# Kernel optimization log

Measured on AMD Instinct MI355X. Metric: run time of the kernel, lower is better.

Reference implementation:

```python
import jax, jax.numpy as jnp
import numpy as np

B, K, L, D, H, DFF, E = 4, 1024, 32, 128, 8, 512, 16384


def setup_inputs() -> dict:
    key = jax.random.key(0)
    ks = jax.random.split(key, 16)
    p = lambda k, sh: (jax.random.normal(k, sh, jnp.float32) * 0.02)
    return {
        "x": jax.random.normal(ks[0], (B, K, L, D), jnp.float32),
        "edge_index": jax.random.randint(ks[1], (B, 2, E), 0, K, jnp.int32),
        "edge_weight": jax.random.uniform(ks[2], (B, E), jnp.float32),
        "w_qkv": p(ks[3], (3 * D, D)), "b_qkv": p(ks[4], (3 * D,)),
        "w_out": p(ks[5], (D, D)), "b_out": p(ks[6], (D,)),
        "w1": p(ks[7], (DFF, D)), "b1": p(ks[8], (DFF,)),
        "w2": p(ks[9], (D, DFF)), "b2": p(ks[10], (D,)),
        "ln1_g": jnp.ones((D,), jnp.float32), "ln1_b": jnp.zeros((D,), jnp.float32),
        "ln2_g": jnp.ones((D,), jnp.float32), "ln2_b": jnp.zeros((D,), jnp.float32),
        "gcn_w": p(ks[11], (D, D)), "gcn_b": p(ks[12], (D,)),
    }


def _ln(x, g, b, eps=1e-5):
    m = x.mean(-1, keepdims=True)
    v = ((x - m) ** 2).mean(-1, keepdims=True)
    return (x - m) * jax.lax.rsqrt(v + eps) * g + b


def reference(x, edge_index, edge_weight, w_qkv, b_qkv, w_out, b_out,
              w1, b1, w2, b2, ln1_g, ln1_b, ln2_g, ln2_b, gcn_w, gcn_b):
    Bx, Kx, Lx, Dx = x.shape
    dh = Dx // H
    h = x.reshape(Bx * Kx, Lx, Dx)                       # [N, L, D], N = B*K
    # --- post-norm TransformerEncoderLayer (self-attn + FFN, relu, dropout=0) ---
    qkv = h @ w_qkv.T + b_qkv
    q, k_, v = jnp.split(qkv, 3, axis=-1)
    q = q.reshape(-1, Lx, H, dh)
    k_ = k_.reshape(-1, Lx, H, dh)
    v = v.reshape(-1, Lx, H, dh)
    scores = jnp.einsum('nlhd,nmhd->nhlm', q, k_) / np.float32(np.sqrt(dh))
    attn = jax.nn.softmax(scores, axis=-1)
    o = jnp.einsum('nhlm,nmhd->nlhd', attn, v).reshape(-1, Lx, Dx)
    o = o @ w_out.T + b_out
    h = _ln(h + o, ln1_g, ln1_b)
    ff = jax.nn.relu(h @ w1.T + b1) @ w2.T + b2
    h = _ln(h + ff, ln2_g, ln2_b)
    xt = h.reshape(Bx, Kx, Lx, Dx)
    # --- GCNConv (sym-normalized, self-loops) applied per (b, l) slice; batched over L ---
    self_idx = jnp.arange(Kx, dtype=edge_index.dtype)

    def gcn_one(xb, ei, ew):                              # xb [K, L, D]
        hh = xb @ gcn_w.T                                 # X W
        row = jnp.concatenate([ei[0], self_idx])          # sources (+ self loops)
        col = jnp.concatenate([ei[1], self_idx])          # targets
        w = jnp.concatenate([ew, jnp.ones((Kx,), ew.dtype)])
        deg = jax.ops.segment_sum(w, col, num_segments=Kx)
        deg_safe = jnp.where(deg > 0, deg, 1.0)
        dinv = jnp.where(deg > 0, jax.lax.rsqrt(deg_safe), 0.0)
        norm = dinv[row] * w * dinv[col]                  # [E+K]
        msg = hh[row] * norm[:, None, None]               # gather + scale
        return jax.ops.segment_sum(msg, col, num_segments=Kx) + gcn_b

    g = jax.vmap(gcn_one)(xt, edge_index, edge_weight)
    return xt + g
```

## Files before the change

kernel.cpp:

```cpp
#include <hip/hip_runtime.h>
#include <hip/hip_bf16.h>

#define BDIM 4
#define KDIM 1024
#define EDIM 16384
#define NSEQ (BDIM * KDIM)
#define REG  25856
#define MOFF 9216

typedef unsigned short ushort_t;
typedef unsigned int   uint32;

typedef __bf16 bf16x8 __attribute__((ext_vector_type(8)));
typedef float  f32x4  __attribute__((ext_vector_type(4)));

#define MFMA(A, B, C) __builtin_amdgcn_mfma_f32_16x16x32_bf16((A), (B), (C), 0, 0, 0)
#define PRIO_HI() __builtin_amdgcn_s_setprio(1)
#define PRIO_LO() __builtin_amdgcn_s_setprio(0)

__device__ __forceinline__ float bf2f(uint32 u) {
    union { uint32 i; float f; } v; v.i = u << 16; return v.f;
}
__device__ __forceinline__ ushort_t f2bf(float f) {
    union { float f; uint32 i; } v; v.f = f;
    uint32 r = (v.i + 0x7fffu + ((v.i >> 16) & 1u)) >> 16;
    return (ushort_t)r;
}
__device__ __forceinline__ uint32 cvtpk(float a, float b) {
    uint32 r;
    asm("v_cvt_pk_bf16_f32 %0, %1, %2" : "=v"(r) : "v"(a), "v"(b));
    return r;
}
__device__ __forceinline__ ushort_t f2bf_hw(float f) { return (ushort_t)cvtpk(f, f); }

__device__ __forceinline__ void unpack8(uint4 v, float* dst) {
    const uint32* pv = (const uint32*)&v;
#pragma unroll
    for (int q = 0; q < 4; q++) {
        uint32 w = pv[q];
        dst[2 * q]     = bf2f(w & 0xffffu);
        dst[2 * q + 1] = bf2f(w >> 16);
    }
}
__device__ __forceinline__ void store16bf(ushort_t* p, const float* v) {
    uint32 w[8];
#pragma unroll
    for (int q = 0; q < 8; q++) w[q] = cvtpk(v[2 * q], v[2 * q + 1]);
    ((uint4*)p)[0] = make_uint4(w[0], w[1], w[2], w[3]);
    ((uint4*)p)[1] = make_uint4(w[4], w[5], w[6], w[7]);
}

#define NWCVT 212992
__global__ void k_prep(const float* __restrict__ wq, const float* __restrict__ wo,
                       const float* __restrict__ w1, const float* __restrict__ w2,
                       const float* __restrict__ wg, ushort_t* __restrict__ dst,
                       float* __restrict__ deg, int* __restrict__ count) {
    int i = blockIdx.x * 256 + threadIdx.x;
    if (i >= NWCVT) return;
    if (i < BDIM * KDIM) { deg[i] = 1.0f; count[i] = 0; }
    float v;
    if      (i <  49152) v = wq[i];
    else if (i <  65536) v = wo[i - 49152];
    else if (i < 131072) v = w1[i - 65536];
    else if (i < 196608) v = w2[i - 131072];
    else                 v = wg[i - 196608];
    dst[i] = f2bf(v);
}

__global__ __launch_bounds__(256)
void k_transformer(const float* __restrict__ x,
                   const ushort_t* __restrict__ wq_bf, const float* __restrict__ b_qkv,
                   const ushort_t* __restrict__ wo_bf, const float* __restrict__ b_out,
                   const ushort_t* __restrict__ w1_bf, const float* __restrict__ b1,
                   const ushort_t* __restrict__ w2_bf, const float* __restrict__ b2,
                   const ushort_t* __restrict__ wg_bf,
                   const float* __restrict__ ln1g, const float* __restrict__ ln1b,
                   const float* __restrict__ ln2g, const float* __restrict__ ln2b,
                   float* __restrict__ out_xt, ushort_t* __restrict__ hh)
{
    const int n0   = blockIdx.x * 2;
    const int tid  = threadIdx.x;
    const int wave = tid >> 6;
    const int lane = tid & 63;
    const int lh   = lane & 15;
    const int lg   = lane >> 4;
    const int l    = tid >> 3;
    const int ds   = (tid & 7) * 16;

    __shared__ __align__(16) char smem[2 * REG];
#define SH(s)  ((ushort_t*)(smem + (s) * REG))
#define SVT(s) ((ushort_t*)(smem + (s) * REG))
#define SM(s)  ((ushort_t*)(smem + (s) * REG + MOFF))
#define SMF(s) ((float*)(smem + (s) * REG + MOFF))

#pragma unroll
    for (int s = 0; s < 2; s++) {
        const float4* px = (const float4*)(x + (size_t)(n0 + s) * 4096 + tid * 16);
        float h0[16];
#pragma unroll
        for (int q = 0; q < 4; q++) {
            float4 v = px[q];
            h0[4 * q] = v.x; h0[4 * q + 1] = v.y; h0[4 * q + 2] = v.z; h0[4 * q + 3] = v.w;
        }
        store16bf(SH(s) + l * 136 + ds, h0);
    }
    __syncthreads();

    {
        bf16x8 af[2][2][4];
#pragma unroll
        for (int s = 0; s < 2; s++)
#pragma unroll
            for (int mt = 0; mt < 2; mt++)
#pragma unroll
                for (int kk = 0; kk < 4; kk++)
                    af[s][mt][kk] = *(const bf16x8*)(SH(s) + (mt * 16 + lh) * 136 + kk * 32 + lg * 8);
        __syncthreads();

        const int ntb = wave * 6;
        float biasv[6];
#pragma unroll
        for (int j = 0; j < 6; j++) biasv[j] = b_qkv[(ntb + j) * 16 + lh];
#pragma unroll
        for (int j = 0; j < 6; j++) {
            bf16x8 bw[4];
#pragma unroll
            for (int kk = 0; kk < 4; kk++)
                bw[kk] = *(const bf16x8*)(wq_bf + (size_t)((ntb + j) * 16 + lh) * 128 + kk * 32 + lg * 8);
            f32x4 A[2][2];
#pragma unroll
            for (int s = 0; s < 2; s++) { A[s][0] = f32x4{0.f,0.f,0.f,0.f}; A[s][1] = f32x4{0.f,0.f,0.f,0.f}; }
            PRIO_HI();
#pragma unroll
            for (int kk = 0; kk < 4; kk++) {
#pragma unroll
                for (int s = 0; s < 2; s++) {
                    A[s][0] = MFMA(af[s][0][kk], bw[kk], A[s][0]);
                    A[s][1] = MFMA(af[s][1][kk], bw[kk], A[s][1]);
                }
            }
            PRIO_LO();
            const int nt  = ntb + j;
            const int col = nt * 16 + lh;
            const float bias = biasv[j];
#pragma unroll
            for (int s = 0; s < 2; s++) {
                if (nt < 16) {
                    const int r0 = lg * 4;
#pragma unroll
                    for (int i = 0; i < 4; i++) {
                        SM(s)[(r0 + i) * 260 + col]      = f2bf_hw(A[s][0][i] + bias);
                        SM(s)[(16 + r0 + i) * 260 + col] = f2bf_hw(A[s][1][i] + bias);
                    }
                } else {
                    const int vc = col - 256;
                    uint32 p01 = cvtpk(A[s][0][0] + bias, A[s][0][1] + bias);
                    uint32 p23 = cvtpk(A[s][0][2] + bias, A[s][0][3] + bias);
                    uint32 q01 = cvtpk(A[s][1][0] + bias, A[s][1][1] + bias);
                    uint32 q23 = cvtpk(A[s][1][2] + bias, A[s][1][3] + bias);
                    *(uint32*)&SVT(s)[vc * 36 + lg * 4]          = p01;
                    *(uint32*)&SVT(s)[vc * 36 + lg * 4 + 2]      = p23;
                    *(uint32*)&SVT(s)[vc * 36 + 16 + lg * 4]     = q01;
                    *(uint32*)&SVT(s)[vc * 36 + 16 + lg * 4 + 2] = q23;
                }
            }
        }
    }
    __syncthreads();

    {
        bf16x8 wbo[2][4];
#pragma unroll
        for (int j = 0; j < 2; j++)
#pragma unroll
            for (int kk = 0; kk < 4; kk++)
                wbo[j][kk] = *(const bf16x8*)(wo_bf + (size_t)((wave * 2 + j) * 16 + lh) * 128 + kk * 32 + lg * 8);
        float bo0 = b_out[(wave * 2 + 0) * 16 + lh];
        float bo1 = b_out[(wave * 2 + 1) * 16 + lh];

#pragma unroll
        for (int s = 0; s < 2; s++) {
            f32x4 sA[2][2][2];
            bf16x8 bz = {};
            PRIO_HI();
#pragma unroll
            for (int hd = 0; hd < 2; hd++) {
                const int h8 = wave * 2 + hd;
#pragma unroll
                for (int mt = 0; mt < 2; mt++) {
                    bf16x8 aq = *(const bf16x8*)(SM(s) + (mt * 16 + lh) * 260 + h8 * 16 + (lg & 1) * 8);
#pragma unroll
                    for (int nt = 0; nt < 2; nt++) {
                        bf16x8 bk = bz;
                        if (lg < 2)
                            bk = *(const bf16x8*)(SM(s) + (nt * 16 + lh) * 260 + 128 + h8 * 16 + lg * 8);
                        f32x4 z = {0.f,0.f,0.f,0.f};
                        sA[hd][mt][nt] = MFMA(aq, bk, z);
                    }
                }
            }
            PRIO_LO();
#pragma unroll
            for (int hd = 0; hd < 2; hd++) {
                const int cb = hd ? (128 + wave * 32) : (wave * 32);
#pragma unroll
                for (int mt = 0; mt < 2; mt++) {
#pragma unroll
                    for (int i = 0; i < 4; i++) {
                        float e0 = __expf(sA[hd][mt][0][i] * 0.25f);
                        float e1 = __expf(sA[hd][mt][1][i] * 0.25f);
                        float sm = e0 + e1;
                        sm += __shfl_xor(sm, 1); sm += __shfl_xor(sm, 2);
                        sm += __shfl_xor(sm, 4); sm += __shfl_xor(sm, 8);
                        float inv = 1.0f / sm;
                        const int row = mt * 16 + lg * 4 + i;
                        SM(s)[row * 260 + cb + lh]      = f2bf_hw(e0 * inv);
                        SM(s)[row * 260 + cb + 16 + lh] = f2bf_hw(e1 * inv);
                    }
                }
            }
            PRIO_HI();
#pragma unroll
            for (int hd = 0; hd < 2; hd++) {
                const int h8 = wave * 2 + hd;
                const int cb = hd ? (128 + wave * 32) : (wave * 32);
                bf16x8 bv = *(const bf16x8*)(SVT(s) + (h8 * 16 + lh) * 36 + lg * 8);
#pragma unroll
                for (int mt = 0; mt < 2; mt++) {
                    bf16x8 ap = *(const bf16x8*)(SM(s) + (mt * 16 + lh) * 260 + cb + lg * 8);
                    f32x4 z = {0.f,0.f,0.f,0.f};
                    f32x4 o = MFMA(ap, bv, z);
                    const int r0 = mt * 16 + lg * 4, c = h8 * 16 + lh;
#pragma unroll
                    for (int i = 0; i < 4; i++)
                        SM(s)[(r0 + i) * 260 + c] = f2bf_hw(o[i]);
                }
            }
            PRIO_LO();
        }
        __syncthreads();
#pragma unroll
        for (int s = 0; s < 2; s++) {
            bf16x8 af2[2][4];
#pragma unroll
            for (int mt = 0; mt < 2; mt++)
#pragma unroll
                for (int kk = 0; kk < 4; kk++)
                    af2[mt][kk] = *(const bf16x8*)(SM(s) + (mt * 16 + lh) * 260 + kk * 32 + lg * 8);
#pragma unroll
            for (int j = 0; j < 2; j++) {
                f32x4 a0 = {0.f,0.f,0.f,0.f}, a1 = {0.f,0.f,0.f,0.f};
                PRIO_HI();
#pragma unroll
                for (int kk = 0; kk < 4; kk++) {
                    a0 = MFMA(af2[0][kk], wbo[j][kk], a0);
                    a1 = MFMA(af2[1][kk], wbo[j][kk], a1);
                }
                PRIO_LO();
                const int col = (wave * 2 + j) * 16 + lh;
                const float bias = j ? bo1 : bo0;
#pragma unroll
                for (int i = 0; i < 4; i++) {
                    SH(s)[(lg * 4 + i) * 136 + col]      = f2bf_hw(a0[i] + bias);
                    SH(s)[(16 + lg * 4 + i) * 136 + col] = f2bf_hw(a1[i] + bias);
                }
            }
        }
        __syncthreads();
        {
            float g[16], be[16];
            {
                const float4* pg = (const float4*)(ln1g + ds);
                const float4* pb = (const float4*)(ln1b + ds);
#pragma unroll
                for (int q = 0; q < 4; q++) {
                    float4 vg = pg[q], vb = pb[q];
                    g[4*q]=vg.x; g[4*q+1]=vg.y; g[4*q+2]=vg.z; g[4*q+3]=vg.w;
                    be[4*q]=vb.x; be[4*q+1]=vb.y; be[4*q+2]=vb.z; be[4*q+3]=vb.w;
                }
            }
#pragma unroll
            for (int s = 0; s < 2; s++) {
                const float4* px = (const float4*)(x + (size_t)(n0 + s) * 4096 + tid * 16);
                float4 hx0 = px[0], hx1 = px[1], hx2 = px[2], hx3 = px[3];
                float h0v[16];
                { float4 v = hx0; h0v[0]=v.x; h0v[1]=v.y; h0v[2]=v.z; h0v[3]=v.w; }
                { float4 v = hx1; h0v[4]=v.x; h0v[5]=v.y; h0v[6]=v.z; h0v[7]=v.w; }
                { float4 v = hx2; h0v[8]=v.x; h0v[9]=v.y; h0v[10]=v.z; h0v[11]=v.w; }
                { float4 v = hx3; h0v[12]=v.x; h0v[13]=v.y; h0v[14]=v.z; h0v[15]=v.w; }
                float t[16]; float sum = 0.f;
#pragma unroll
                for (int i = 0; i < 16; i++) {
                    t[i] = h0v[i] + bf2f((uint32)SH(s)[l * 136 + ds + i]);
                    sum += t[i];
                }
                sum += __shfl_xor(sum, 1); sum += __shfl_xor(sum, 2); sum += __shfl_xor(sum, 4);
                float mean = sum * (1.f / 128.f);
                float vs = 0.f;
#pragma unroll
                for (int i = 0; i < 16; i++) { float d = t[i] - mean; vs += d * d; }
                vs += __shfl_xor(vs, 1); vs += __shfl_xor(vs, 2); vs += __shfl_xor(vs, 4);
                float rs = rsqrtf(vs * (1.f / 128.f) + 1e-5f);
                float h1v[16];
#pragma unroll
                for (int i = 0; i < 16; i++)
                    h1v[i] = (t[i] - mean) * rs * g[i] + be[i];
                store16bf(SH(s) + l * 136 + ds, h1v);
            }
        }
    }
    __syncthreads();

    f32x4 fa[2][4];
#pragma unroll
    for (int s = 0; s < 2; s++)
#pragma unroll
        for (int q = 0; q < 4; q++) fa[s][q] = f32x4{0.f,0.f,0.f,0.f};
    const int col0 = wave * 32 + lh, col1 = col0 + 16;
#pragma unroll
    for (int r = 0; r < 2; r++) {
#pragma unroll
        for (int s = 0; s < 2; s++) {
            bf16x8 ah[2][4];
#pragma unroll
            for (int mt = 0; mt < 2; mt++)
#pragma unroll
                for (int kk = 0; kk < 4; kk++)
                    ah[mt][kk] = *(const bf16x8*)(SH(s) + (mt * 16 + lh) * 136 + kk * 32 + lg * 8);
            float b1v[4];
#pragma unroll
            for (int j = 0; j < 4; j++) b1v[j] = b1[(r * 16 + wave * 4 + j) * 16 + lh];
#pragma unroll
            for (int j = 0; j < 4; j++) {
                bf16x8 bw[4];
                {
                    const int nt = (r * 16 + wave * 4 + j) * 16 + lh;
#pragma unroll
                    for (int kk = 0; kk < 4; kk++)
                        bw[kk] = *(const bf16x8*)(w1_bf + (size_t)nt * 128 + kk * 32 + lg * 8);
                }
                f32x4 a0 = {0.f,0.f,0.f,0.f}, a1 = {0.f,0.f,0.f,0.f};
                PRIO_HI();
#pragma unroll
                for (int kk = 0; kk < 4; kk++) {
                    a0 = MFMA(ah[0][kk], bw[kk], a0);
                    a1 = MFMA(ah[1][kk], bw[kk], a1);
                }
                PRIO_LO();
                const float bias = b1v[j];
                const int cl = (wave * 4 + j) * 16 + lh;
                const int r0 = lg * 4;
#pragma unroll
                for (int i = 0; i < 4; i++) {
                    SM(s)[(r0 + i) * 260 + cl]      = f2bf_hw(fmaxf(a0[i] + bias, 0.f));
                    SM(s)[(16 + r0 + i) * 260 + cl] = f2bf_hw(fmaxf(a1[i] + bias, 0.f));
                }
            }
        }
        __syncthreads();
#pragma unroll
        for (int kk = 0; kk < 8; kk++) {
            bf16x8 wp0 = *(const bf16x8*)(w2_bf + (size_t)col0 * 512 + r * 256 + kk * 32 + lg * 8);
            bf16x8 wp1 = *(const bf16x8*)(w2_bf + (size_t)col1 * 512 + r * 256 + kk * 32 + lg * 8);
            PRIO_HI();
#pragma unroll
            for (int s = 0; s < 2; s++) {
                bf16x8 a0 = *(const bf16x8*)(SM(s) + lh * 260 + kk * 32 + lg * 8);
                bf16x8 a1 = *(const bf16x8*)(SM(s) + (16 + lh) * 260 + kk * 32 + lg * 8);
                fa[s][0] = MFMA(a0, wp0, fa[s][0]);
                fa[s][1] = MFMA(a1, wp0, fa[s][1]);
                fa[s][2] = MFMA(a0, wp1, fa[s][2]);
                fa[s][3] = MFMA(a1, wp1, fa[s][3]);
            }
            PRIO_LO();
        }
        __syncthreads();
    }
    {
        const float bi0 = b2[col0], bi1 = b2[col1];
#pragma unroll
        for (int s = 0; s < 2; s++) {
#pragma unroll
            for (int i = 0; i < 4; i++) {
                SMF(s)[(lg * 4 + i) * 130 + col0]      = fa[s][0][i] + bi0;
                SMF(s)[(16 + lg * 4 + i) * 130 + col0] = fa[s][1][i] + bi0;
                SMF(s)[(lg * 4 + i) * 130 + col1]      = fa[s][2][i] + bi1;
                SMF(s)[(16 + lg * 4 + i) * 130 + col1] = fa[s][3][i] + bi1;
            }
        }
    }
    __syncthreads();

    {
        float g[16], be[16];
        {
            const float4* pg = (const float4*)(ln2g + ds);
            const float4* pb = (const float4*)(ln2b + ds);
#pragma unroll
            for (int q = 0; q < 4; q++) {
                float4 vg = pg[q], vb = pb[q];
                g[4*q]=vg.x; g[4*q+1]=vg.y; g[4*q+2]=vg.z; g[4*q+3]=vg.w;
                be[4*q]=vb.x; be[4*q+1]=vb.y; be[4*q+2]=vb.z; be[4*q+3]=vb.w;
            }
        }
#pragma unroll
        for (int s = 0; s < 2; s++) {
            float t[16]; float sum = 0.f;
#pragma unroll
            for (int i = 0; i < 16; i++) {
                t[i] = bf2f((uint32)SH(s)[l * 136 + ds + i]) + SMF(s)[l * 130 + ds + i];
                sum += t[i];
            }
            sum += __shfl_xor(sum, 1); sum += __shfl_xor(sum, 2); sum += __shfl_xor(sum, 4);
            float mean = sum * (1.f / 128.f);
            float vs = 0.f;
#pragma unroll
            for (int i = 0; i < 16; i++) { float d = t[i] - mean; vs += d * d; }
            vs += __shfl_xor(vs, 1); vs += __shfl_xor(vs, 2); vs += __shfl_xor(vs, 4);
            float rs = rsqrtf(vs * (1.f / 128.f) + 1e-5f);
            float h2v[16];
#pragma unroll
            for (int i = 0; i < 16; i++)
                h2v[i] = (t[i] - mean) * rs * g[i] + be[i];
            float4* po = (float4*)(out_xt + (size_t)(n0 + s) * 4096 + tid * 16);
#pragma unroll
            for (int q = 0; q < 4; q++)
                po[q] = make_float4(h2v[4 * q], h2v[4 * q + 1], h2v[4 * q + 2], h2v[4 * q + 3]);
            store16bf(SH(s) + l * 136 + ds, h2v);
        }
    }
    __syncthreads();

    {
        bf16x8 wb[2][4];
#pragma unroll
        for (int j = 0; j < 2; j++)
#pragma unroll
            for (int kk = 0; kk < 4; kk++)
                wb[j][kk] = *(const bf16x8*)(wg_bf + (size_t)((wave * 2 + j) * 16 + lh) * 128 + kk * 32 + lg * 8);
#pragma unroll
        for (int s = 0; s < 2; s++) {
            bf16x8 ag[2][4];
#pragma unroll
            for (int mt = 0; mt < 2; mt++)
#pragma unroll
                for (int kk = 0; kk < 4; kk++)
                    ag[mt][kk] = *(const bf16x8*)(SH(s) + (mt * 16 + lh) * 136 + kk * 32 + lg * 8);
            ushort_t* hp = hh + (size_t)(n0 + s) * 4096;
#pragma unroll
            for (int j = 0; j < 2; j++) {
                f32x4 a0 = {0.f,0.f,0.f,0.f}, a1 = {0.f,0.f,0.f,0.f};
                PRIO_HI();
#pragma unroll
                for (int kk = 0; kk < 4; kk++) {
                    a0 = MFMA(ag[0][kk], wb[j][kk], a0);
                    a1 = MFMA(ag[1][kk], wb[j][kk], a1);
                }
                PRIO_LO();
                const int col = (wave * 2 + j) * 16 + lh;
                const int r0 = lg * 4;
#pragma unroll
                for (int i = 0; i < 4; i++) {
                    hp[(r0 + i) * 128 + col]      = f2bf_hw(a0[i]);
                    hp[(16 + r0 + i) * 128 + col] = f2bf_hw(a1[i]);
                }
            }
        }
    }
#undef SH
#undef SVT
#undef SM
#undef SMF
}

__global__ void k_degcount(const int* __restrict__ ei, const float* __restrict__ ew,
                           float* deg, int* count) {
    int idx = blockIdx.x * 256 + threadIdx.x;
    if (idx >= BDIM * EDIM) return;
    int b = idx / EDIM, e = idx - b * EDIM;
    int col = ei[(size_t)b * 2 * EDIM + EDIM + e];
    float w = ew[(size_t)b * EDIM + e];
    atomicAdd(&deg[b * KDIM + col], w);
    atomicAdd(&count[b * KDIM + col], 1);
}

__global__ __launch_bounds__(1024)
void k_scan(const int* __restrict__ count, int* offs, int* cursor) {
    __shared__ int s[KDIM];
    int b = blockIdx.x, i = threadIdx.x;
    int c = count[b * KDIM + i];
    s[i] = c; __syncthreads();
#pragma unroll 1
    for (int off = 1; off < KDIM; off <<= 1) {
        int t = (i >= off) ? s[i - off] : 0;
        __syncthreads();
        s[i] += t;
        __syncthreads();
    }
    int excl = s[i] - c;
    offs[b * KDIM + i] = excl;
    cursor[b * KDIM + i] = excl;
}

__global__ void k_fill(const int* __restrict__ ei, int* cursor, int* elist) {
    int idx = blockIdx.x * 256 + threadIdx.x;
    if (idx >= BDIM * EDIM) return;
    int b = idx / EDIM, e = idx - b * EDIM;
    int col = ei[(size_t)b * 2 * EDIM + EDIM + e];
    int pos = atomicAdd(&cursor[b * KDIM + col], 1);
    elist[(size_t)b * EDIM + pos] = e;
}

__global__ __launch_bounds__(256)
void k_gather(const int* __restrict__ ei, const float* __restrict__ ew,
              const float* __restrict__ deg, const int* __restrict__ offs,
              const int* __restrict__ count, const int* __restrict__ elist,
              const ushort_t* __restrict__ hh, const float* __restrict__ gcn_b,
              float* __restrict__ out)
{
    const int node = blockIdx.x;
    const int b = node >> 10, i = node & 1023;
    const int tid = threadIdx.x;
    const float dcol = rsqrtf(deg[node]);
    const int off = offs[node], cnt = count[node];
    const ushort_t* hhb = hh + ((size_t)b * KDIM) * 4096;
    const int* elb = elist + (size_t)b * EDIM;
    const int* eib = ei + (size_t)b * 2 * EDIM;
    const float* ewb = ew + (size_t)b * EDIM;
    const float* degb = deg + b * KDIM;

    float acc[16];
    {
        const uint4* ph = (const uint4*)(hhb + (size_t)i * 4096 + tid * 16);
        uint4 a = ph[0], bb = ph[1];
        float tmp[16]; unpack8(a, tmp); unpack8(bb, tmp + 8);
        float nrm = dcol * dcol;
#pragma unroll
        for (int k = 0; k < 16; k++) acc[k] = tmp[k] * nrm;
    }
    if (cnt > 0) {
        int rowA, rowB = 0; float wA, wB = 0.f;
        {
            int eA = elb[off];
            rowA = eib[eA]; wA = ewb[eA];
            if (cnt > 1) { int eB = elb[off + 1]; rowB = eib[eB]; wB = ewb[eB]; }
        }
        for (int t = 0; t < cnt; t += 2) {
            const bool hasB = (t + 1 < cnt);
            const uint4* pA = (const uint4*)(hhb + (size_t)rowA * 4096 + tid * 16);
            uint4 a0 = pA[0], a1 = pA[1];
            uint4 b0 = make_uint4(0, 0, 0, 0), b1 = make_uint4(0, 0, 0, 0);
            if (hasB) {
                const uint4* pB = (const uint4*)(hhb + (size_t)rowB * 4096 + tid * 16);
                b0 = pB[0]; b1 = pB[1];
            }
            float nA = rsqrtf(degb[rowA]) * wA * dcol;
            float nB = hasB ? rsqrtf(degb[rowB]) * wB * dcol : 0.f;
            int rA2 = 0, rB2 = 0; float wA2 = 0.f, wB2 = 0.f;
            if (t + 2 < cnt) { int e = elb[off + t + 2]; rA2 = eib[e]; wA2 = ewb[e]; }
            if (t + 3 < cnt) { int e = elb[off + t + 3]; rB2 = eib[e]; wB2 = ewb[e]; }
            float tA[16]; unpack8(a0, tA); unpack8(a1, tA + 8);
#pragma unroll
            for (int k = 0; k < 16; k++) acc[k] += tA[k] * nA;
            float tB[16]; unpack8(b0, tB); unpack8(b1, tB + 8);
#pragma unroll
            for (int k = 0; k < 16; k++) acc[k] += tB[k] * nB;
            rowA = rA2; wA = wA2; rowB = rB2; wB = wB2;
        }
    }
    const int d0 = (tid * 16) & 127;
    float4* po = (float4*)(out + (size_t)node * 4096 + tid * 16);
#pragma unroll
    for (int q = 0; q < 4; q++) {
        float4 xo = po[q];
        xo.x += acc[4 * q]     + gcn_b[d0 + 4 * q];
        xo.y += acc[4 * q + 1] + gcn_b[d0 + 4 * q + 1];
        xo.z += acc[4 * q + 2] + gcn_b[d0 + 4 * q + 2];
        xo.w += acc[4 * q + 3] + gcn_b[d0 + 4 * q + 3];
        po[q] = xo;
    }
}

extern "C" void kernel_launch(void* const* d_in, const int* in_sizes, int n_in,
                              void* d_out, int out_size, void* d_ws, size_t ws_size,
                              hipStream_t stream) {
    const float* x     = (const float*)d_in[0];
    const int*   ei    = (const int*)d_in[1];
    const float* ew    = (const float*)d_in[2];
    const float* w_qkv = (const float*)d_in[3];
    const float* b_qkv = (const float*)d_in[4];
    const float* w_out = (const float*)d_in[5];
    const float* b_out = (const float*)d_in[6];
    const float* w1    = (const float*)d_in[7];
    const float* b1    = (const float*)d_in[8];
    const float* w2    = (const float*)d_in[9];
    const float* b2    = (const float*)d_in[10];
    const float* ln1g  = (const float*)d_in[11];
    const float* ln1b  = (const float*)d_in[12];
    const float* ln2g  = (const float*)d_in[13];
    const float* ln2b  = (const float*)d_in[14];
    const float* gcnw  = (const float*)d_in[15];
    const float* gcnb  = (const float*)d_in[16];
    float* out = (float*)d_out;

    char* ws = (char*)d_ws;
    ushort_t* wbf   = (ushort_t*)ws;
    ushort_t* wq_bf = wbf;
    ushort_t* wo_bf = wbf + 49152;
    ushort_t* w1_bf = wbf + 65536;
    ushort_t* w2_bf = wbf + 131072;
    ushort_t* wg_bf = wbf + 196608;
    float*    deg   = (float*)(ws + 425984);
    int*      count = (int*)(ws + 442368);
    int*      offs  = (int*)(ws + 458752);
    int*      cursor= (int*)(ws + 475136);
    int*      elist = (int*)(ws + 491520);
    ushort_t* hh    = (ushort_t*)(ws + 753664);

    k_prep<<<(NWCVT + 255) / 256, 256, 0, stream>>>(w_qkv, w_out, w1, w2, gcnw, wbf, deg, count);
    k_transformer<<<NSEQ / 2, 256, 0, stream>>>(x, wq_bf, b_qkv, wo_bf, b_out,
                                                w1_bf, b1, w2_bf, b2, wg_bf,
                                                ln1g, ln1b, ln2g, ln2b, out, hh);
    k_degcount<<<256, 256, 0, stream>>>(ei, ew, deg, count);
    k_scan<<<BDIM, 1024, 0, stream>>>(count, offs, cursor);
    k_fill<<<256, 256, 0, stream>>>(ei, cursor, elist);
    k_gather<<<NSEQ, 256, 0, stream>>>(ei, ew, deg, offs, count, elist, hh, gcnb, out);
}
```

Measured before the change: 291.1 us.

## Fuse graph degree, scan and CSR fill into one LDS-atomic kernel

Replaces the three graph-preprocessing kernels (degree/count with global atomics, scan, fill) with a single per-batch kernel that does the degree and count accumulation, prefix scan and edge-list fill in shared memory. The degree init also moves out of k_prep. This removes two launches and the global atomic traffic. The trade-off is that only 4 blocks run this stage, so it is serial per batch, although it is small.

```diff
diff --git a/kernel.cpp b/kernel.cpp
--- a/kernel.cpp
+++ b/kernel.cpp
@@ -53,11 +53,9 @@
 #define NWCVT 212992
 __global__ void k_prep(const float* __restrict__ wq, const float* __restrict__ wo,
                        const float* __restrict__ w1, const float* __restrict__ w2,
-                       const float* __restrict__ wg, ushort_t* __restrict__ dst,
-                       float* __restrict__ deg, int* __restrict__ count) {
+                       const float* __restrict__ wg, ushort_t* __restrict__ dst) {
     int i = blockIdx.x * 256 + threadIdx.x;
     if (i >= NWCVT) return;
-    if (i < BDIM * KDIM) { deg[i] = 1.0f; count[i] = 0; }
     float v;
     if      (i <  49152) v = wq[i];
     else if (i <  65536) v = wo[i - 49152];
@@ -65,6 +63,55 @@
     else if (i < 196608) v = w2[i - 131072];
     else                 v = wg[i - 196608];
     dst[i] = f2bf(v);
+}
+
+__global__ __launch_bounds__(1024)
+void k_graph(const int* __restrict__ ei, const float* __restrict__ ew,
+             float* __restrict__ deg, int* __restrict__ count,
+             int* __restrict__ offs, int* __restrict__ elist)
+{
+    const int b = blockIdx.x, i = threadIdx.x;
+    __shared__ float degL[KDIM];
+    __shared__ int   cntL[KDIM];
+    __shared__ int   curL[KDIM];
+    __shared__ int   sc[KDIM];
+    const int* colb = ei + (size_t)b * 2 * EDIM + EDIM;
+    const float* ewb = ew + (size_t)b * EDIM;
+
+    degL[i] = 1.0f;
+    cntL[i] = 0;
+    __syncthreads();
+#pragma unroll
+    for (int it = 0; it < EDIM / KDIM; it++) {
+        const int e = it * KDIM + i;
+        const int col = colb[e];
+        atomicAdd(&degL[col], ewb[e]);
+        atomicAdd(&cntL[col], 1);
+    }
+    __syncthreads();
+    const int c = cntL[i];
+    sc[i] = c;
+    __syncthreads();
+#pragma unroll 1
+    for (int off = 1; off < KDIM; off <<= 1) {
+        int t = (i >= off) ? sc[i - off] : 0;
+        __syncthreads();
+        sc[i] += t;
+        __syncthreads();
+    }
+    const int excl = sc[i] - c;
+    curL[i] = excl;
+    deg[b * KDIM + i]   = degL[i];
+    count[b * KDIM + i] = c;
+    offs[b * KDIM + i]  = excl;
+    __syncthreads();
+#pragma unroll
+    for (int it = 0; it < EDIM / KDIM; it++) {
+        const int e = it * KDIM + i;
+        const int col = colb[e];
+        const int pos = atomicAdd(&curL[col], 1);
+        elist[(size_t)b * EDIM + pos] = e;
+    }
 }
 
 __global__ __launch_bounds__(256)
@@ -471,44 +518,6 @@
 #undef SVT
 #undef SM
 #undef SMF
-}
-
-__global__ void k_degcount(const int* __restrict__ ei, const float* __restrict__ ew,
-                           float* deg, int* count) {
-    int idx = blockIdx.x * 256 + threadIdx.x;
-    if (idx >= BDIM * EDIM) return;
-    int b = idx / EDIM, e = idx - b * EDIM;
-    int col = ei[(size_t)b * 2 * EDIM + EDIM + e];
-    float w = ew[(size_t)b * EDIM + e];
-    atomicAdd(&deg[b * KDIM + col], w);
-    atomicAdd(&count[b * KDIM + col], 1);
-}
-
-__global__ __launch_bounds__(1024)
-void k_scan(const int* __restrict__ count, int* offs, int* cursor) {
-    __shared__ int s[KDIM];
-    int b = blockIdx.x, i = threadIdx.x;
-    int c = count[b * KDIM + i];
-    s[i] = c; __syncthreads();
-#pragma unroll 1
-    for (int off = 1; off < KDIM; off <<= 1) {
-        int t = (i >= off) ? s[i - off] : 0;
-        __syncthreads();
-        s[i] += t;
-        __syncthreads();
-    }
-    int excl = s[i] - c;
-    offs[b * KDIM + i] = excl;
-    cursor[b * KDIM + i] = excl;
-}
-
-__global__ void k_fill(const int* __restrict__ ei, int* cursor, int* elist) {
-    int idx = blockIdx.x * 256 + threadIdx.x;
-    if (idx >= BDIM * EDIM) return;
-    int b = idx / EDIM, e = idx - b * EDIM;
-    int col = ei[(size_t)b * 2 * EDIM + EDIM + e];
-    int pos = atomicAdd(&cursor[b * KDIM + col], 1);
-    elist[(size_t)b * EDIM + pos] = e;
 }
 
 __global__ __launch_bounds__(256)
@@ -613,16 +622,13 @@
     float*    deg   = (float*)(ws + 425984);
     int*      count = (int*)(ws + 442368);
     int*      offs  = (int*)(ws + 458752);
-    int*      cursor= (int*)(ws + 475136);
     int*      elist = (int*)(ws + 491520);
     ushort_t* hh    = (ushort_t*)(ws + 753664);
 
-    k_prep<<<(NWCVT + 255) / 256, 256, 0, stream>>>(w_qkv, w_out, w1, w2, gcnw, wbf, deg, count);
+    k_prep<<<(NWCVT + 255) / 256, 256, 0, stream>>>(w_qkv, w_out, w1, w2, gcnw, wbf);
+    k_graph<<<BDIM, 1024, 0, stream>>>(ei, ew, deg, count, offs, elist);
     k_transformer<<<NSEQ / 2, 256, 0, stream>>>(x, wq_bf, b_qkv, wo_bf, b_out,
                                                 w1_bf, b1, w2_bf, b2, wg_bf,
                                                 ln1g, ln1b, ln2g, ln2b, out, hh);
-    k_degcount<<<256, 256, 0, stream>>>(ei, ew, deg, count);
-    k_scan<<<BDIM, 1024, 0, stream>>>(count, offs, cursor);
-    k_fill<<<256, 256, 0, stream>>>(ei, cursor, elist);
     k_gather<<<NSEQ, 256, 0, stream>>>(ei, ew, deg, offs, count, elist, hh, gcnb, out);
 }
```

Result: slower. 310.5 us (+6.7%).
